# Kernel tuning notes

Measured on AMD Instinct MI355X. Metric: run time of the kernel, lower is better.

The kernel has to match this reference:

```python
import jax, jax.numpy as jnp
import numpy as np

S, B, H = 2048, 32, 1024

def setup_inputs() -> dict:
    key = jax.random.key(0)
    k1, k2, k3, k4 = jax.random.split(key, 4)
    scale = 1.0 / np.sqrt(H)
    hidden = jax.random.normal(k1, (B, H), dtype=jnp.float32)
    encoder_outputs = jax.random.normal(k2, (S, B, H), dtype=jnp.float32)
    W = jax.random.normal(k3, (H, H), dtype=jnp.float32) * scale  # nn.Linear weight [out,in]
    b = jax.random.normal(k4, (H,), dtype=jnp.float32) * scale    # nn.Linear bias
    return {"hidden": hidden, "encoder_outputs": encoder_outputs, "W": W, "b": b}

def reference(hidden, encoder_outputs, W, b):
    # method == 'general': energy[s,b] = W @ encoder_outputs[s,b] + b
    # score[b,s] = hidden[b] . energy[s,b]
    energy = jnp.einsum('sbh,oh->sbo', encoder_outputs, W) + b  # [S,B,H]
    attn_energies = jnp.einsum('bh,sbh->bs', hidden, energy)    # [B,S]
    # F.softmax on a 2D tensor defaults to dim=1 (over seq)
    attn = jax.nn.softmax(attn_energies, axis=1)
    return attn[:, None, :]  # [B,1,S]
```

## Files before the change

kernel.cpp:

```cpp
#include <hip/hip_runtime.h>
#include <math.h>

#define SS 2048
#define BB 32
#define HH 1024

__global__ __launch_bounds__(256) void vmat_kernel(const float* __restrict__ hidden,
                                                   const float* __restrict__ W,
                                                   float* __restrict__ v) {
    const int h = blockIdx.x * 256 + threadIdx.x;
    const int b = blockIdx.y;
    const float* __restrict__ hrow = hidden + b * HH;
    float a0 = 0.f, a1 = 0.f, a2 = 0.f, a3 = 0.f;
    for (int o = 0; o < HH; o += 4) {
        a0 = fmaf(hrow[o + 0], W[(size_t)(o + 0) * HH + h], a0);
        a1 = fmaf(hrow[o + 1], W[(size_t)(o + 1) * HH + h], a1);
        a2 = fmaf(hrow[o + 2], W[(size_t)(o + 2) * HH + h], a2);
        a3 = fmaf(hrow[o + 3], W[(size_t)(o + 3) * HH + h], a3);
    }
    v[b * HH + h] = (a0 + a1) + (a2 + a3);
}

__global__ __launch_bounds__(256) void score_kernel(const float* __restrict__ enc,
                                                    const float* __restrict__ v,
                                                    float* __restrict__ out) {
    const int b = blockIdx.y;
    const int wave = threadIdx.x >> 6;
    const int lane = threadIdx.x & 63;

    const float4* __restrict__ vrow = (const float4*)(v + (size_t)b * HH);
    const float4 v0 = vrow[lane];
    const float4 v1 = vrow[lane + 64];
    const float4 v2 = vrow[lane + 128];
    const float4 v3 = vrow[lane + 192];

    const int s_base = blockIdx.x * 16 + wave * 4;
    #pragma unroll
    for (int i = 0; i < 4; ++i) {
        const int s = s_base + i;
        const float4* __restrict__ erow =
            (const float4*)(enc + (size_t)s * (BB * HH) + (size_t)b * HH);
        const float4 e0 = erow[lane];
        const float4 e1 = erow[lane + 64];
        const float4 e2 = erow[lane + 128];
        const float4 e3 = erow[lane + 192];

        float acc = 0.f;
        acc = fmaf(e0.x, v0.x, acc); acc = fmaf(e0.y, v0.y, acc);
        acc = fmaf(e0.z, v0.z, acc); acc = fmaf(e0.w, v0.w, acc);
        acc = fmaf(e1.x, v1.x, acc); acc = fmaf(e1.y, v1.y, acc);
        acc = fmaf(e1.z, v1.z, acc); acc = fmaf(e1.w, v1.w, acc);
        acc = fmaf(e2.x, v2.x, acc); acc = fmaf(e2.y, v2.y, acc);
        acc = fmaf(e2.z, v2.z, acc); acc = fmaf(e2.w, v2.w, acc);
        acc = fmaf(e3.x, v3.x, acc); acc = fmaf(e3.y, v3.y, acc);
        acc = fmaf(e3.z, v3.z, acc); acc = fmaf(e3.w, v3.w, acc);

        #pragma unroll
        for (int off = 32; off >= 1; off >>= 1)
            acc += __shfl_xor(acc, off, 64);

        if (lane == 0) out[(size_t)b * SS + s] = acc;
    }
}

__global__ __launch_bounds__(256) void softmax_kernel(float* __restrict__ out) {
    const int b = blockIdx.x;
    float* __restrict__ row = out + (size_t)b * SS;
    const int tid = threadIdx.x;
    const int wave = tid >> 6;
    const int lane = tid & 63;

    float x[8];
    float m = -INFINITY;
    #pragma unroll
    for (int i = 0; i < 8; ++i) {
        x[i] = row[tid + 256 * i];
        m = fmaxf(m, x[i]);
    }
    #pragma unroll
    for (int off = 32; off >= 1; off >>= 1)
        m = fmaxf(m, __shfl_xor(m, off, 64));

    __shared__ float redm[4];
    __shared__ float reds[4];
    if (lane == 0) redm[wave] = m;
    __syncthreads();
    m = fmaxf(fmaxf(redm[0], redm[1]), fmaxf(redm[2], redm[3]));

    float ssum = 0.f;
    #pragma unroll
    for (int i = 0; i < 8; ++i) {
        x[i] = expf(x[i] - m);
        ssum += x[i];
    }
    #pragma unroll
    for (int off = 32; off >= 1; off >>= 1)
        ssum += __shfl_xor(ssum, off, 64);
    if (lane == 0) reds[wave] = ssum;
    __syncthreads();
    ssum = (reds[0] + reds[1]) + (reds[2] + reds[3]);

    const float inv = 1.0f / ssum;
    #pragma unroll
    for (int i = 0; i < 8; ++i)
        row[tid + 256 * i] = x[i] * inv;
}

extern "C" void kernel_launch(void* const* d_in, const int* in_sizes, int n_in,
                              void* d_out, int out_size, void* d_ws, size_t ws_size,
                              hipStream_t stream) {
    const float* hidden = (const float*)d_in[0];
    const float* enc    = (const float*)d_in[1];
    const float* W      = (const float*)d_in[2];
    float* out = (float*)d_out;
    float* v   = (float*)d_ws;

    vmat_kernel<<<dim3(HH / 256, BB), 256, 0, stream>>>(hidden, W, v);
    score_kernel<<<dim3(SS / 16, BB), 256, 0, stream>>>(enc, v, out);
    softmax_kernel<<<BB, 256, 0, stream>>>(out);
}
```

Baseline: 406.7 us.

## Split vmat reduction across output chunks and use nontemporal encoder loads

The hidden-times-W product is split into 8 partial sums over chunks of the reduction dimension. Each thread loads float4 rows of W, which gives more independent memory traffic per thread. The score kernel adds the 8 partial vectors as it loads v. Encoder outputs are read with nontemporal loads to avoid polluting the cache with streamed data. The cost is extra workspace and 8 partial-vector reads per score block; the bias-free path and the algebra are unchanged.

```diff
diff --git a/kernel.cpp b/kernel.cpp
--- a/kernel.cpp
+++ b/kernel.cpp
@@ -4,46 +4,60 @@
 #define SS 2048
 #define BB 32
 #define HH 1024
+#define OCH 8
+#define OLEN (HH/OCH)
+
+typedef float v4f __attribute__((ext_vector_type(4)));
 
 __global__ __launch_bounds__(256) void vmat_kernel(const float* __restrict__ hidden,
                                                    const float* __restrict__ W,
-                                                   float* __restrict__ v) {
-    const int h = blockIdx.x * 256 + threadIdx.x;
-    const int b = blockIdx.y;
-    const float* __restrict__ hrow = hidden + b * HH;
-    float a0 = 0.f, a1 = 0.f, a2 = 0.f, a3 = 0.f;
-    for (int o = 0; o < HH; o += 4) {
-        a0 = fmaf(hrow[o + 0], W[(size_t)(o + 0) * HH + h], a0);
-        a1 = fmaf(hrow[o + 1], W[(size_t)(o + 1) * HH + h], a1);
-        a2 = fmaf(hrow[o + 2], W[(size_t)(o + 2) * HH + h], a2);
-        a3 = fmaf(hrow[o + 3], W[(size_t)(o + 3) * HH + h], a3);
+                                                   float* __restrict__ vpart) {
+    const int oc = blockIdx.x;
+    const int b  = blockIdx.y;
+    const int t  = threadIdx.x;
+    const float* __restrict__ hrow = hidden + (size_t)b * HH;
+    const v4f* __restrict__ Wrow = (const v4f*)W;
+
+    v4f acc = (v4f){0.f, 0.f, 0.f, 0.f};
+    const int o0 = oc * OLEN;
+    #pragma unroll 4
+    for (int oo = 0; oo < OLEN; ++oo) {
+        const int o = o0 + oo;
+        const float hs = hrow[o];
+        const v4f w = Wrow[(size_t)o * 256 + t];
+        acc += hs * w;
     }
-    v[b * HH + h] = (a0 + a1) + (a2 + a3);
+    ((v4f*)(vpart + ((size_t)oc * BB + b) * HH))[t] = acc;
 }
 
 __global__ __launch_bounds__(256) void score_kernel(const float* __restrict__ enc,
-                                                    const float* __restrict__ v,
+                                                    const float* __restrict__ vpart,
                                                     float* __restrict__ out) {
     const int b = blockIdx.y;
     const int wave = threadIdx.x >> 6;
     const int lane = threadIdx.x & 63;
 
-    const float4* __restrict__ vrow = (const float4*)(v + (size_t)b * HH);
-    const float4 v0 = vrow[lane];
-    const float4 v1 = vrow[lane + 64];
-    const float4 v2 = vrow[lane + 128];
-    const float4 v3 = vrow[lane + 192];
+    v4f v0 = (v4f){0.f,0.f,0.f,0.f}, v1 = v0, v2 = v0, v3 = v0;
+    #pragma unroll
+    for (int c = 0; c < OCH; ++c) {
+        const v4f* __restrict__ vrow =
+            (const v4f*)(vpart + ((size_t)c * BB + b) * HH);
+        v0 += vrow[lane];
+        v1 += vrow[lane + 64];
+        v2 += vrow[lane + 128];
+        v3 += vrow[lane + 192];
+    }
 
     const int s_base = blockIdx.x * 16 + wave * 4;
     #pragma unroll
     for (int i = 0; i < 4; ++i) {
         const int s = s_base + i;
-        const float4* __restrict__ erow =
-            (const float4*)(enc + (size_t)s * (BB * HH) + (size_t)b * HH);
-        const float4 e0 = erow[lane];
-        const float4 e1 = erow[lane + 64];
-        const float4 e2 = erow[lane + 128];
-        const float4 e3 = erow[lane + 192];
+        const v4f* __restrict__ erow =
+            (const v4f*)(enc + (size_t)s * (BB * HH) + (size_t)b * HH);
+        const v4f e0 = __builtin_nontemporal_load(&erow[lane]);
+        const v4f e1 = __builtin_nontemporal_load(&erow[lane + 64]);
+        const v4f e2 = __builtin_nontemporal_load(&erow[lane + 128]);
+        const v4f e3 = __builtin_nontemporal_load(&erow[lane + 192]);
 
         float acc = 0.f;
         acc = fmaf(e0.x, v0.x, acc); acc = fmaf(e0.y, v0.y, acc);
@@ -112,10 +126,10 @@
     const float* hidden = (const float*)d_in[0];
     const float* enc    = (const float*)d_in[1];
     const float* W      = (const float*)d_in[2];
-    float* out = (float*)d_out;
-    float* v   = (float*)d_ws;
+    float* out   = (float*)d_out;
+    float* vpart = (float*)d_ws;
 
-    vmat_kernel<<<dim3(HH / 256, BB), 256, 0, stream>>>(hidden, W, v);
-    score_kernel<<<dim3(SS / 16, BB), 256, 0, stream>>>(enc, v, out);
+    vmat_kernel<<<dim3(OCH, BB), 256, 0, stream>>>(hidden, W, vpart);
+    score_kernel<<<dim3(SS / 16, BB), 256, 0, stream>>>(enc, vpart, out);
     softmax_kernel<<<BB, 256, 0, stream>>>(out);
 }
```

New measurement: 369.5 us. -9.2%, faster.
